# Performance work log

Hardware: AMD Instinct MI355X
Metric: run time of the kernel (lower is better)

The kernel has to match this reference:

```python
import jax, jax.numpy as jnp
import numpy as np

L = 2048   # query seq len
S = 2048   # key/value seq len
N = 1      # batch (pytorch 3D attn_mask of shape (H,L,S) requires N*H==H -> N=1)
E = 2048   # embed_dim
H = 16     # num_heads


def setup_inputs() -> dict:
    rng = jax.random.key(0)
    ks = jax.random.split(rng, 8)
    g = lambda k, sh, sc: jax.random.normal(k, sh, jnp.float32) * sc
    return {
        "query": jax.random.normal(ks[0], (L, N, E), jnp.float32),
        "key": jax.random.normal(ks[1], (S, N, E), jnp.float32),
        "value": jax.random.normal(ks[2], (S, N, E), jnp.float32),
        "time_emb": jax.random.normal(ks[3], (S, E), jnp.float32),
        # nn.MultiheadAttention params
        "in_proj_w": g(ks[4], (3 * E, E), 0.02),
        "in_proj_b": jnp.zeros((3 * E,), jnp.float32),
        "out_w": g(ks[5], (E, E), 0.02),
        "out_b": jnp.zeros((E,), jnp.float32),
        # time_proj: Linear(E -> H)
        "tp_w": g(ks[6], (H, E), 0.02),
        "tp_b": jnp.zeros((H,), jnp.float32),
        # LayerNorm
        "ln_g": jnp.ones((E,), jnp.float32),
        "ln_b": jnp.zeros((E,), jnp.float32),
    }


def reference(query, key, value, time_emb, in_proj_w, in_proj_b, out_w, out_b,
              tp_w, tp_b, ln_g, ln_b):
    Lq, Nb, Ed = query.shape
    Hh = tp_w.shape[0]
    Dh = Ed // Hh
    wq, wk, wv = jnp.split(in_proj_w, 3, axis=0)
    bq, bk, bv = jnp.split(in_proj_b, 3)
    q = (query @ wq.T + bq).reshape(Lq, Nb, Hh, Dh)
    k = (key @ wk.T + bk).reshape(-1, Nb, Hh, Dh)
    v = (value @ wv.T + bv).reshape(-1, Nb, Hh, Dh)
    scale = 1.0 / np.sqrt(Dh).astype(np.float32)
    # per-head additive time bias: (H, S), broadcast over query positions
    time_bias = (time_emb @ tp_w.T + tp_b).T  # (H, S)
    scores = jnp.einsum('lnhd,snhd->nhls', q, k) * scale
    scores = scores + time_bias[None, :, None, :]  # (N,H,L,S)
    attn = jax.nn.softmax(scores, axis=-1)
    ctx = jnp.einsum('nhls,snhd->lnhd', attn, v).reshape(Lq, Nb, Ed)
    attn_output = ctx @ out_w.T + out_b
    # residual + LayerNorm (eps=1e-5)
    x = query + attn_output
    mu = x.mean(axis=-1, keepdims=True)
    var = ((x - mu) ** 2).mean(axis=-1, keepdims=True)
    return (x - mu) / jnp.sqrt(var + 1e-5) * ln_g + ln_b
```

## Files before the change

### kernel.cpp

```cpp
#include <hip/hip_runtime.h>
#include <math.h>

#define L_DIM 2048
#define S_DIM 2048
#define E_DIM 2048
#define H_DIM 16
#define D_HEAD 128

using bf16x8 = __attribute__((ext_vector_type(8))) short;
using f32x4  = __attribute__((ext_vector_type(4))) float;

__device__ __forceinline__ unsigned pack2_bf16(float a, float b) {
  unsigned ua = __builtin_bit_cast(unsigned, a) + 0x8000u;
  unsigned ub = __builtin_bit_cast(unsigned, b) + 0x8000u;
  return __builtin_amdgcn_perm(ub, ua, 0x07060302u);
}
__device__ __forceinline__ unsigned short f2bf(float a) {
  unsigned u = __builtin_bit_cast(unsigned, a) + 0x8000u;
  return (unsigned short)(u >> 16);
}
__device__ __forceinline__ float bflo(unsigned u) {
  return __builtin_bit_cast(float, u << 16);
}
__device__ __forceinline__ float bfhi(unsigned u) {
  return __builtin_bit_cast(float, u & 0xffff0000u);
}

__device__ __forceinline__ void gl_lds16(const unsigned short* g, unsigned short* l) {
  __builtin_amdgcn_global_load_lds(
      (const __attribute__((address_space(1))) void*)g,
      (__attribute__((address_space(3))) void*)l, 16, 0, 0);
}

#define FA_SFT 23.083120654223414f
#define FA_C1  0.12752977f

__global__ __launch_bounds__(256)
void convert_bf16(const float* __restrict__ q, const float* __restrict__ k,
                  const float* __restrict__ v, const float* __restrict__ w_in,
                  const float* __restrict__ w_out,
                  unsigned short* __restrict__ qa, unsigned short* __restrict__ ka,
                  unsigned short* __restrict__ va, unsigned short* __restrict__ wqkv,
                  unsigned short* __restrict__ wo)
{
  const int z = blockIdx.y;
  const float* src;
  unsigned short* dst;
  switch (z) {
    case 0: src = q; dst = qa; break;
    case 1: src = k; dst = ka; break;
    case 2: src = v; dst = va; break;
    case 3: src = w_in;           dst = wqkv;           break;
    case 4: src = w_in + 4194304; dst = wqkv + 4194304; break;
    case 5: src = w_in + 8388608; dst = wqkv + 8388608; break;
    default: src = w_out; dst = wo; break;
  }
  size_t i = ((size_t)blockIdx.x * 256 + threadIdx.x) * 8;
  float4 a = *(const float4*)(src + i);
  float4 b = *(const float4*)(src + i + 4);
  uint4 o;
  o.x = pack2_bf16(a.x, a.y);
  o.y = pack2_bf16(a.z, a.w);
  o.z = pack2_bf16(b.x, b.y);
  o.w = pack2_bf16(b.z, b.w);
  *(uint4*)(dst + i) = o;
}

#define GBM 128
#define GBN 128
#define GBK 32

template<int MODE>
__global__ __launch_bounds__(256, 2)
void gemm_bt(const unsigned short* __restrict__ Aq, const unsigned short* __restrict__ Ak,
             const unsigned short* __restrict__ Av, const unsigned short* __restrict__ Bmat,
             const float* __restrict__ bias0,
             unsigned short* __restrict__ qb, unsigned short* __restrict__ kb,
             unsigned short* __restrict__ vt,
             const float* __restrict__ Res, float* __restrict__ Xout,
             float* __restrict__ Xout2)
{
  __shared__ unsigned short As[GBM * GBK];
  __shared__ unsigned short Bs[GBN * GBK];
  const int tid  = threadIdx.x;
  const int lane = tid & 63;
  const int wave = tid >> 6;
  const int quad = lane >> 4;
  const int c16  = lane & 15;
  const int m0 = blockIdx.y * GBM;
  const int n0 = blockIdx.x * GBN;
  const int z  = blockIdx.z;

  const unsigned short* A;
  const unsigned short* B;
  const float* bias;
  int kbeg, kend;
  if (MODE == 0) {
    A = (z == 0) ? Aq : (z == 1) ? Ak : Av;
    B = Bmat + (size_t)z * E_DIM * E_DIM;
    bias = bias0 + z * E_DIM;
    kbeg = 0; kend = E_DIM;
  } else {
    A = Aq; B = Bmat; bias = bias0;
    kbeg = z * 1024; kend = kbeg + 1024;
  }

  const int ar = lane >> 2;
  const int sg = (ar ^ (ar >> 2)) & 3;
  const int ac = (lane & 3) ^ sg;
  const unsigned short* aG0 = A + (size_t)(m0 + wave * 16 + ar) * E_DIM + kbeg + ac * 8;
  const unsigned short* aG1 = aG0 + (size_t)64 * E_DIM;
  const unsigned short* bG0 = B + (size_t)(n0 + wave * 16 + ar) * E_DIM + kbeg + ac * 8;
  const unsigned short* bG1 = bG0 + (size_t)64 * E_DIM;
  unsigned short* aS0 = &As[wave * 512];
  unsigned short* aS1 = &As[(wave + 4) * 512];
  unsigned short* bS0 = &Bs[wave * 512];
  unsigned short* bS1 = &Bs[(wave + 4) * 512];

  const int sigm = (c16 ^ (c16 >> 2)) & 3;
  const int fr = (4 * c16 + (quad ^ sigm)) * 8;

  f32x4 acc[4][4];
#pragma unroll
  for (int i = 0; i < 4; i++)
#pragma unroll
    for (int j = 0; j < 4; j++) acc[i][j] = (f32x4){0.f, 0.f, 0.f, 0.f};

  const int wm = (wave >> 1) * 64;
  const int wn = (wave & 1) * 64;
  const int ga = (wm >> 4);
  const int gb = (wn >> 4);

  for (int k0 = kbeg; k0 < kend; k0 += GBK) {
    __syncthreads();
    gl_lds16(aG0, aS0);
    gl_lds16(aG1, aS1);
    gl_lds16(bG0, bS0);
    gl_lds16(bG1, bS1);
    aG0 += GBK; aG1 += GBK; bG0 += GBK; bG1 += GBK;
    __syncthreads();

    bf16x8 af[4], bfr[4];
#pragma unroll
    for (int t = 0; t < 4; t++) {
      af[t]  = *(const bf16x8*)&As[(ga + t) * 512 + fr];
      bfr[t] = *(const bf16x8*)&Bs[(gb + t) * 512 + fr];
    }
#pragma unroll
    for (int tm = 0; tm < 4; tm++)
#pragma unroll
      for (int tn = 0; tn < 4; tn++)
        acc[tm][tn] = __builtin_amdgcn_mfma_f32_16x16x32_bf16(af[tm], bfr[tn],
                                                              acc[tm][tn], 0, 0, 0);
  }

  float bv[4];
#pragma unroll
  for (int tn = 0; tn < 4; tn++) bv[tn] = bias[n0 + wn + tn * 16 + c16];

  if (MODE == 1) {
    if (z == 0) {
#pragma unroll
      for (int tm = 0; tm < 4; tm++) {
        int mr = m0 + wm + tm * 16 + quad * 4;
#pragma unroll
        for (int tn = 0; tn < 4; tn++) {
          int n = n0 + wn + tn * 16 + c16;
#pragma unroll
          for (int r = 0; r < 4; r++) {
            size_t idx = (size_t)(mr + r) * E_DIM + n;
            Xout[idx] = acc[tm][tn][r] + bv[tn] + Res[idx];
          }
        }
      }
    } else {
#pragma unroll
      for (int tm = 0; tm < 4; tm++) {
        int mr = m0 + wm + tm * 16 + quad * 4;
#pragma unroll
        for (int tn = 0; tn < 4; tn++) {
          int n = n0 + wn + tn * 16 + c16;
#pragma unroll
          for (int r = 0; r < 4; r++)
            Xout2[(size_t)(mr + r) * E_DIM + n] = acc[tm][tn][r];
        }
      }
    }
  } else if (z < 2) {
    unsigned short* O = (z == 0) ? qb : kb;
#pragma unroll
    for (int tm = 0; tm < 4; tm++) {
      int mr = m0 + wm + tm * 16 + quad * 4;
#pragma unroll
      for (int tn = 0; tn < 4; tn++) {
        int n = n0 + wn + tn * 16 + c16;
#pragma unroll
        for (int r = 0; r < 4; r++)
          O[(size_t)(mr + r) * E_DIM + n] = f2bf(acc[tm][tn][r] + bv[tn]);
      }
    }
  } else {
#pragma unroll
    for (int tm = 0; tm < 4; tm++) {
      int mr = m0 + wm + tm * 16 + quad * 4;
#pragma unroll
      for (int tn = 0; tn < 4; tn++) {
        int n = n0 + wn + tn * 16 + c16;
        uint2 pv;
        pv.x = pack2_bf16(acc[tm][tn][0] + bv[tn], acc[tm][tn][1] + bv[tn]);
        pv.y = pack2_bf16(acc[tm][tn][2] + bv[tn], acc[tm][tn][3] + bv[tn]);
        *(uint2*)(vt + (size_t)n * S_DIM + mr) = pv;
      }
    }
  }
}

__global__ __launch_bounds__(256)
void time_bias_kernel(const float* __restrict__ temb, const float* __restrict__ tpw,
                      const float* __restrict__ tpb, float* __restrict__ tb)
{
  const int lane = threadIdx.x & 63;
  const int wave = threadIdx.x >> 6;
  const int s = blockIdx.x * 4 + wave;
  float acc[16];
#pragma unroll
  for (int hh = 0; hh < 16; hh++) acc[hh] = 0.f;
  for (int i = 0; i < 32; i++) {
    int e = lane + i * 64;
    float t = temb[(size_t)s * E_DIM + e];
#pragma unroll
    for (int hh = 0; hh < 16; hh++)
      acc[hh] = fmaf(t, tpw[hh * E_DIM + e], acc[hh]);
  }
#pragma unroll
  for (int hh = 0; hh < 16; hh++) {
#pragma unroll
    for (int d = 1; d < 64; d <<= 1)
      acc[hh] += __shfl_xor(acc[hh], d, 64);
  }
#pragma unroll
  for (int hh = 0; hh < 16; hh++)
    if (lane == hh)
      tb[(size_t)hh * S_DIM + s] = (acc[hh] + tpb[hh]) * 1.44269504f - FA_SFT;
}

__global__ __launch_bounds__(256, 4)
void flash_attn(const unsigned short* __restrict__ qb,
                const unsigned short* __restrict__ kb,
                const unsigned short* __restrict__ vt,
                const float* __restrict__ tb,
                unsigned short* __restrict__ Opart,
                float* __restrict__ lsum)
{
  __shared__ unsigned short Ks[64 * 128];
  __shared__ unsigned short Vs[128 * 64];
  __shared__ unsigned short Ps[64 * 64];

  const int tid  = threadIdx.x;
  const int lane = tid & 63;
  const int wave = tid >> 6;
  const int quad = lane >> 4;
  const int c16  = lane & 15;
  const int h     = blockIdx.y;
  const int z     = blockIdx.z;
  const int lrow0 = blockIdx.x * 64 + wave * 16;
  const int sbase = z * 1024;

  bf16x8 qf[4];
#pragma unroll
  for (int kd = 0; kd < 4; kd++)
    qf[kd] = *(const bf16x8*)(qb + (size_t)(lrow0 + c16) * E_DIM + h * D_HEAD
                              + kd * 32 + quad * 8);

  const int krow = tid >> 4;
  const int kc   = tid & 15;
  const int vrow = tid >> 3;
  const int vc   = tid & 7;
  const unsigned short* kg = kb + (size_t)(sbase + krow) * E_DIM + h * D_HEAD + kc * 8;
  const unsigned short* vg = vt + (size_t)(h * D_HEAD + vrow) * S_DIM + sbase + vc * 8;
  const int kslot = (kc ^ krow) * 8;
  const int vslot = (vc ^ (vrow & 7)) * 8;
  const float* tbh = tb + (size_t)h * S_DIM + sbase;

  f32x4 of[8];
#pragma unroll
  for (int i = 0; i < 8; i++) of[i] = (f32x4){0.f, 0.f, 0.f, 0.f};
  float li4[4] = {0.f, 0.f, 0.f, 0.f};

  bf16x8 kreg[4], vreg[4];
#pragma unroll
  for (int i = 0; i < 4; i++) kreg[i] = *(const bf16x8*)(kg + (size_t)i * 16 * E_DIM);
#pragma unroll
  for (int i = 0; i < 4; i++) vreg[i] = *(const bf16x8*)(vg + (size_t)i * 32 * S_DIM);

  const int prow = (wave * 16 + c16) * 64;
  const int k7   = c16 & 7;

  for (int ch = 0; ch < 16; ch++) {
    __syncthreads();
#pragma unroll
    for (int i = 0; i < 4; i++)
      *(bf16x8*)&Ks[(krow + 16 * i) * 128 + kslot] = kreg[i];
#pragma unroll
    for (int i = 0; i < 4; i++)
      *(bf16x8*)&Vs[(vrow + 32 * i) * 64 + vslot] = vreg[i];
    __syncthreads();

    if (ch < 15) {
      const unsigned short* kg2 = kg + (size_t)(ch + 1) * 64 * E_DIM;
      const unsigned short* vg2 = vg + (ch + 1) * 64;
#pragma unroll
      for (int i = 0; i < 4; i++) kreg[i] = *(const bf16x8*)(kg2 + (size_t)i * 16 * E_DIM);
#pragma unroll
      for (int i = 0; i < 4; i++) vreg[i] = *(const bf16x8*)(vg2 + (size_t)i * 32 * S_DIM);
    }

    float4 bb[4];
#pragma unroll
    for (int tn = 0; tn < 4; tn++)
      bb[tn] = *(const float4*)(tbh + ch * 64 + tn * 16 + quad * 4);

    f32x4 sc[4];
#pragma unroll
    for (int tn = 0; tn < 4; tn++) sc[tn] = (f32x4){0.f, 0.f, 0.f, 0.f};
#pragma unroll
    for (int tn = 0; tn < 4; tn++)
#pragma unroll
      for (int kd = 0; kd < 4; kd++) {
        bf16x8 kf = *(const bf16x8*)&Ks[(tn * 16 + c16) * 128
                                        + (((kd * 4 + quad) ^ c16) << 3)];
        sc[tn] = __builtin_amdgcn_mfma_f32_16x16x32_bf16(kf, qf[kd], sc[tn], 0, 0, 0);
      }

#pragma unroll
    for (int tn = 0; tn < 4; tn++) {
      float p0 = exp2f(fmaf(sc[tn][0], FA_C1, bb[tn].x));
      float p1 = exp2f(fmaf(sc[tn][1], FA_C1, bb[tn].y));
      float p2 = exp2f(fmaf(sc[tn][2], FA_C1, bb[tn].z));
      float p3 = exp2f(fmaf(sc[tn][3], FA_C1, bb[tn].w));
      li4[tn] += (p0 + p1) + (p2 + p3);
      uint2 pv;
      pv.x = pack2_bf16(p0, p1);
      pv.y = pack2_bf16(p2, p3);
      int p8 = (((tn * 2 + (quad >> 1)) ^ k7) << 1) | (quad & 1);
      *(uint2*)&Ps[prow + p8 * 4] = pv;
    }

#pragma unroll
    for (int ks = 0; ks < 2; ks++) {
      int po = ((ks * 4 + quad) ^ k7) << 3;
      bf16x8 ap = *(const bf16x8*)&Ps[prow + po];
#pragma unroll
      for (int td = 0; td < 8; td++) {
        bf16x8 vf = *(const bf16x8*)&Vs[(td * 16 + c16) * 64 + po];
        of[td] = __builtin_amdgcn_mfma_f32_16x16x32_bf16(ap, vf, of[td], 0, 0, 0);
      }
    }
  }

  float lt = (li4[0] + li4[1]) + (li4[2] + li4[3]);
  lt += __shfl_xor(lt, 16, 64);
  lt += __shfl_xor(lt, 32, 64);
  if (quad == 0)
    lsum[(size_t)z * 32768 + (size_t)h * 2048 + lrow0 + c16] = lt;

#pragma unroll
  for (int r = 0; r < 4; r++) {
    size_t lrow = lrow0 + quad * 4 + r;
#pragma unroll
    for (int td = 0; td < 8; td++)
      Opart[((size_t)z * 2048 + lrow) * 2048 + h * D_HEAD + td * 16 + c16] =
          f2bf(of[td][r]);
  }
}

__global__ __launch_bounds__(256)
void combine_kernel(const unsigned short* __restrict__ Opart,
                    const float* __restrict__ lsum,
                    unsigned short* __restrict__ ctx)
{
  size_t i = ((size_t)blockIdx.x * 256 + threadIdx.x) * 8;
  int l = (int)(i >> 11);
  int e = (int)(i & 2047);
  int h = e >> 7;
  float inv = 1.0f / (lsum[h * 2048 + l] + lsum[32768 + h * 2048 + l]);
  uint4 a = *(const uint4*)(Opart + i);
  uint4 b = *(const uint4*)(Opart + 4194304 + i);
  uint4 o;
  o.x = pack2_bf16((bflo(a.x) + bflo(b.x)) * inv, (bfhi(a.x) + bfhi(b.x)) * inv);
  o.y = pack2_bf16((bflo(a.y) + bflo(b.y)) * inv, (bfhi(a.y) + bfhi(b.y)) * inv);
  o.z = pack2_bf16((bflo(a.z) + bflo(b.z)) * inv, (bfhi(a.z) + bfhi(b.z)) * inv);
  o.w = pack2_bf16((bflo(a.w) + bflo(b.w)) * inv, (bfhi(a.w) + bfhi(b.w)) * inv);
  *(uint4*)(ctx + i) = o;
}

__global__ __launch_bounds__(256)
void layernorm_kernel(const float* __restrict__ x0, const float* __restrict__ x1,
                      const float* __restrict__ g, const float* __restrict__ b,
                      float* __restrict__ out)
{
  const int row = blockIdx.x;
  const int tid = threadIdx.x;
  const int lane = tid & 63, wave = tid >> 6;
  const float* xr0 = x0 + (size_t)row * E_DIM;
  const float* xr1 = x1 + (size_t)row * E_DIM;
  float4 a0 = *(const float4*)(xr0 + tid * 4);
  float4 a1 = *(const float4*)(xr0 + 1024 + tid * 4);
  float4 c0 = *(const float4*)(xr1 + tid * 4);
  float4 c1 = *(const float4*)(xr1 + 1024 + tid * 4);
  float4 v0 = {a0.x + c0.x, a0.y + c0.y, a0.z + c0.z, a0.w + c0.w};
  float4 v1 = {a1.x + c1.x, a1.y + c1.y, a1.z + c1.z, a1.w + c1.w};
  float s  = v0.x + v0.y + v0.z + v0.w + v1.x + v1.y + v1.z + v1.w;
  float ss = v0.x*v0.x + v0.y*v0.y + v0.z*v0.z + v0.w*v0.w
           + v1.x*v1.x + v1.y*v1.y + v1.z*v1.z + v1.w*v1.w;
#pragma unroll
  for (int d = 1; d < 64; d <<= 1) {
    s  += __shfl_xor(s, d, 64);
    ss += __shfl_xor(ss, d, 64);
  }
  __shared__ float red[8];
  if (lane == 0) { red[wave] = s; red[wave + 4] = ss; }
  __syncthreads();
  s  = red[0] + red[1] + red[2] + red[3];
  ss = red[4] + red[5] + red[6] + red[7];
  float mu   = s * (1.f / E_DIM);
  float var  = ss * (1.f / E_DIM) - mu * mu;
  float rstd = rsqrtf(var + 1e-5f);

  float4 g0 = *(const float4*)(g + tid * 4);
  float4 b0 = *(const float4*)(b + tid * 4);
  float4 g1 = *(const float4*)(g + 1024 + tid * 4);
  float4 b1 = *(const float4*)(b + 1024 + tid * 4);
  float4 o0, o1;
  o0.x = (v0.x - mu) * rstd * g0.x + b0.x;
  o0.y = (v0.y - mu) * rstd * g0.y + b0.y;
  o0.z = (v0.z - mu) * rstd * g0.z + b0.z;
  o0.w = (v0.w - mu) * rstd * g0.w + b0.w;
  o1.x = (v1.x - mu) * rstd * g1.x + b1.x;
  o1.y = (v1.y - mu) * rstd * g1.y + b1.y;
  o1.z = (v1.z - mu) * rstd * g1.z + b1.z;
  o1.w = (v1.w - mu) * rstd * g1.w + b1.w;
  *(float4*)(out + (size_t)row * E_DIM + tid * 4) = o0;
  *(float4*)(out + (size_t)row * E_DIM + 1024 + tid * 4) = o1;
}

extern "C" void kernel_launch(void* const* d_in, const int* in_sizes, int n_in,
                              void* d_out, int out_size, void* d_ws, size_t ws_size,
                              hipStream_t stream) {
  const float* query     = (const float*)d_in[0];
  const float* key       = (const float*)d_in[1];
  const float* value     = (const float*)d_in[2];
  const float* time_emb  = (const float*)d_in[3];
  const float* in_proj_w = (const float*)d_in[4];
  const float* in_proj_b = (const float*)d_in[5];
  const float* out_w     = (const float*)d_in[6];
  const float* out_b     = (const float*)d_in[7];
  const float* tp_w      = (const float*)d_in[8];
  const float* tp_b      = (const float*)d_in[9];
  const float* ln_g      = (const float*)d_in[10];
  const float* ln_b      = (const float*)d_in[11];

  char* ws = (char*)d_ws;
  unsigned short* qa   = (unsigned short*)(ws + 0);
  unsigned short* ka   = (unsigned short*)(ws + 8388608);
  unsigned short* va   = (unsigned short*)(ws + 16777216);
  unsigned short* wqkv = (unsigned short*)(ws + 25165824);
  unsigned short* wo   = (unsigned short*)(ws + 50331648);
  unsigned short* qb   = (unsigned short*)(ws + 58720256);
  unsigned short* kb   = (unsigned short*)(ws + 67108864);
  unsigned short* vt   = (unsigned short*)(ws + 75497472);
  float*          tb   = (float*)(ws + 83886080);
  unsigned short* Opart = (unsigned short*)(ws + 0);
  float*          lsum  = (float*)(ws + 16777216);
  unsigned short* ctx   = (unsigned short*)(ws + 33554432);
  float*          xb0   = (float*)(ws + 0);
  float*          xb1   = (float*)(ws + 16777216);

  convert_bf16<<<dim3(2048, 7), 256, 0, stream>>>(query, key, value, in_proj_w,
                                                  out_w, qa, ka, va, wqkv, wo);
  time_bias_kernel<<<512, 256, 0, stream>>>(time_emb, tp_w, tp_b, tb);
  gemm_bt<0><<<dim3(16, 16, 3), 256, 0, stream>>>(qa, ka, va, wqkv, in_proj_b,
                                                  qb, kb, vt, nullptr, nullptr,
                                                  nullptr);
  flash_attn<<<dim3(32, 16, 2), 256, 0, stream>>>(qb, kb, vt, tb, Opart, lsum);
  combine_kernel<<<2048, 256, 0, stream>>>(Opart, lsum, ctx);
  gemm_bt<1><<<dim3(16, 16, 2), 256, 0, stream>>>(ctx, nullptr, nullptr, wo,
                                                  out_b, nullptr, nullptr, nullptr,
                                                  query, xb0, xb1);
  layernorm_kernel<<<2048, 256, 0, stream>>>(xb0, xb1, ln_g, ln_b, (float*)d_out);
}
```

Before: 349.3 us.

## Double GEMM K-tile to 64 and fold time-bias kernel into convert launch

The projection GEMMs now stage a 64-wide K slice per iteration instead of 32, using a new 8-way XOR swizzle and twice as many async global-to-LDS loads. Each barrier pair is then followed by two MFMA sub-steps, halving the barrier count per K. The time-bias projection moves into the bf16 conversion kernel as an extra grid slice, removing one kernel launch. LDS use per block doubles to 32 KB, which may limit occupancy, and the new swizzle must stay conflict-free.

```diff
diff --git a/kernel.cpp b/kernel.cpp
--- a/kernel.cpp
+++ b/kernel.cpp
@@ -41,9 +41,38 @@
                   const float* __restrict__ w_out,
                   unsigned short* __restrict__ qa, unsigned short* __restrict__ ka,
                   unsigned short* __restrict__ va, unsigned short* __restrict__ wqkv,
-                  unsigned short* __restrict__ wo)
+                  unsigned short* __restrict__ wo,
+                  const float* __restrict__ temb, const float* __restrict__ tpw,
+                  const float* __restrict__ tpb, float* __restrict__ tb)
 {
   const int z = blockIdx.y;
+  if (z == 7) {
+    if (blockIdx.x >= 512) return;
+    const int lane = threadIdx.x & 63;
+    const int wave = threadIdx.x >> 6;
+    const int s = blockIdx.x * 4 + wave;
+    float acc[16];
+#pragma unroll
+    for (int hh = 0; hh < 16; hh++) acc[hh] = 0.f;
+    for (int i = 0; i < 32; i++) {
+      int e = lane + i * 64;
+      float t = temb[(size_t)s * E_DIM + e];
+#pragma unroll
+      for (int hh = 0; hh < 16; hh++)
+        acc[hh] = fmaf(t, tpw[hh * E_DIM + e], acc[hh]);
+    }
+#pragma unroll
+    for (int hh = 0; hh < 16; hh++) {
+#pragma unroll
+      for (int d = 1; d < 64; d <<= 1)
+        acc[hh] += __shfl_xor(acc[hh], d, 64);
+    }
+#pragma unroll
+    for (int hh = 0; hh < 16; hh++)
+      if (lane == hh)
+        tb[(size_t)hh * S_DIM + s] = (acc[hh] + tpb[hh]) * 1.44269504f - FA_SFT;
+    return;
+  }
   const float* src;
   unsigned short* dst;
   switch (z) {
@@ -68,7 +97,7 @@
 
 #define GBM 128
 #define GBN 128
-#define GBK 32
+#define GBK 64
 
 template<int MODE>
 __global__ __launch_bounds__(256, 2)
@@ -105,20 +134,28 @@
     kbeg = z * 1024; kend = kbeg + 1024;
   }
 
-  const int ar = lane >> 2;
-  const int sg = (ar ^ (ar >> 2)) & 3;
-  const int ac = (lane & 3) ^ sg;
-  const unsigned short* aG0 = A + (size_t)(m0 + wave * 16 + ar) * E_DIM + kbeg + ac * 8;
-  const unsigned short* aG1 = aG0 + (size_t)64 * E_DIM;
-  const unsigned short* bG0 = B + (size_t)(n0 + wave * 16 + ar) * E_DIM + kbeg + ac * 8;
-  const unsigned short* bG1 = bG0 + (size_t)64 * E_DIM;
-  unsigned short* aS0 = &As[wave * 512];
-  unsigned short* aS1 = &As[(wave + 4) * 512];
-  unsigned short* bS0 = &Bs[wave * 512];
-  unsigned short* bS1 = &Bs[(wave + 4) * 512];
-
-  const int sigm = (c16 ^ (c16 >> 2)) & 3;
-  const int fr = (4 * c16 + (quad ^ sigm)) * 8;
+  const int srow = lane >> 3;
+  const int sc   = (lane & 7) ^ srow;
+  const unsigned short* aG00 = A + (size_t)(m0 + wave * 16 + srow) * E_DIM + kbeg + sc * 8;
+  const unsigned short* aG01 = aG00 + (size_t)8 * E_DIM;
+  const unsigned short* aG10 = aG00 + (size_t)64 * E_DIM;
+  const unsigned short* aG11 = aG00 + (size_t)72 * E_DIM;
+  const unsigned short* bG00 = B + (size_t)(n0 + wave * 16 + srow) * E_DIM + kbeg + sc * 8;
+  const unsigned short* bG01 = bG00 + (size_t)8 * E_DIM;
+  const unsigned short* bG10 = bG00 + (size_t)64 * E_DIM;
+  const unsigned short* bG11 = bG00 + (size_t)72 * E_DIM;
+  unsigned short* aS00 = &As[wave * 1024];
+  unsigned short* aS01 = aS00 + 512;
+  unsigned short* aS10 = &As[(wave + 4) * 1024];
+  unsigned short* aS11 = aS10 + 512;
+  unsigned short* bS00 = &Bs[wave * 1024];
+  unsigned short* bS01 = bS00 + 512;
+  unsigned short* bS10 = &Bs[(wave + 4) * 1024];
+  unsigned short* bS11 = bS10 + 512;
+
+  const int k7 = c16 & 7;
+  const int fr0 = (8 * c16 + ((0 * 4 + quad) ^ k7)) * 8;
+  const int fr1 = (8 * c16 + ((1 * 4 + quad) ^ k7)) * 8;
 
   f32x4 acc[4][4];
 #pragma unroll
@@ -133,25 +170,30 @@
 
   for (int k0 = kbeg; k0 < kend; k0 += GBK) {
     __syncthreads();
-    gl_lds16(aG0, aS0);
-    gl_lds16(aG1, aS1);
-    gl_lds16(bG0, bS0);
-    gl_lds16(bG1, bS1);
-    aG0 += GBK; aG1 += GBK; bG0 += GBK; bG1 += GBK;
+    gl_lds16(aG00, aS00); gl_lds16(aG01, aS01);
+    gl_lds16(aG10, aS10); gl_lds16(aG11, aS11);
+    gl_lds16(bG00, bS00); gl_lds16(bG01, bS01);
+    gl_lds16(bG10, bS10); gl_lds16(bG11, bS11);
+    aG00 += GBK; aG01 += GBK; aG10 += GBK; aG11 += GBK;
+    bG00 += GBK; bG01 += GBK; bG10 += GBK; bG11 += GBK;
     __syncthreads();
 
-    bf16x8 af[4], bfr[4];
-#pragma unroll
-    for (int t = 0; t < 4; t++) {
-      af[t]  = *(const bf16x8*)&As[(ga + t) * 512 + fr];
-      bfr[t] = *(const bf16x8*)&Bs[(gb + t) * 512 + fr];
-    }
-#pragma unroll
-    for (int tm = 0; tm < 4; tm++)
-#pragma unroll
-      for (int tn = 0; tn < 4; tn++)
-        acc[tm][tn] = __builtin_amdgcn_mfma_f32_16x16x32_bf16(af[tm], bfr[tn],
-                                                              acc[tm][tn], 0, 0, 0);
+#pragma unroll
+    for (int s = 0; s < 2; s++) {
+      const int fr = s ? fr1 : fr0;
+      bf16x8 af[4], bfr[4];
+#pragma unroll
+      for (int t = 0; t < 4; t++) {
+        af[t]  = *(const bf16x8*)&As[(ga + t) * 1024 + fr];
+        bfr[t] = *(const bf16x8*)&Bs[(gb + t) * 1024 + fr];
+      }
+#pragma unroll
+      for (int tm = 0; tm < 4; tm++)
+#pragma unroll
+        for (int tn = 0; tn < 4; tn++)
+          acc[tm][tn] = __builtin_amdgcn_mfma_f32_16x16x32_bf16(af[tm], bfr[tn],
+                                                                acc[tm][tn], 0, 0, 0);
+    }
   }
 
   float bv[4];
@@ -213,35 +255,6 @@
       }
     }
   }
-}
-
-__global__ __launch_bounds__(256)
-void time_bias_kernel(const float* __restrict__ temb, const float* __restrict__ tpw,
-                      const float* __restrict__ tpb, float* __restrict__ tb)
-{
-  const int lane = threadIdx.x & 63;
-  const int wave = threadIdx.x >> 6;
-  const int s = blockIdx.x * 4 + wave;
-  float acc[16];
-#pragma unroll
-  for (int hh = 0; hh < 16; hh++) acc[hh] = 0.f;
-  for (int i = 0; i < 32; i++) {
-    int e = lane + i * 64;
-    float t = temb[(size_t)s * E_DIM + e];
-#pragma unroll
-    for (int hh = 0; hh < 16; hh++)
-      acc[hh] = fmaf(t, tpw[hh * E_DIM + e], acc[hh]);
-  }
-#pragma unroll
-  for (int hh = 0; hh < 16; hh++) {
-#pragma unroll
-    for (int d = 1; d < 64; d <<= 1)
-      acc[hh] += __shfl_xor(acc[hh], d, 64);
-  }
-#pragma unroll
-  for (int hh = 0; hh < 16; hh++)
-    if (lane == hh)
-      tb[(size_t)hh * S_DIM + s] = (acc[hh] + tpb[hh]) * 1.44269504f - FA_SFT;
 }
 
 __global__ __launch_bounds__(256, 4)
@@ -476,9 +489,9 @@
   float*          xb0   = (float*)(ws + 0);
   float*          xb1   = (float*)(ws + 16777216);
 
-  convert_bf16<<<dim3(2048, 7), 256, 0, stream>>>(query, key, value, in_proj_w,
-                                                  out_w, qa, ka, va, wqkv, wo);
-  time_bias_kernel<<<512, 256, 0, stream>>>(time_emb, tp_w, tp_b, tb);
+  convert_bf16<<<dim3(2048, 8), 256, 0, stream>>>(query, key, value, in_proj_w,
+                                                  out_w, qa, ka, va, wqkv, wo,
+                                                  time_emb, tp_w, tp_b, tb);
   gemm_bt<0><<<dim3(16, 16, 3), 256, 0, stream>>>(qa, ka, va, wqkv, in_proj_b,
                                                   qb, kb, vt, nullptr, nullptr,
                                                   nullptr);
```

After: 362.7 us. 3.8% more time.
